# Kernel optimization log

Measured on AMD Instinct MI355X. Metric: run time of the kernel, lower is better.

The kernel has to match this reference:

```python
import jax, jax.numpy as jnp
import numpy as np

B, C, H, W = 4, 512, 64, 64
C8 = C // 8


def setup_inputs() -> dict:
    key = jax.random.key(0)
    ks = jax.random.split(key, 5)
    s1 = 1.0 / np.sqrt(C)
    return {
        "feat_map": jax.random.normal(ks[0], (B, C, H, W), jnp.float32),
        "w1": jax.random.normal(ks[1], (C8, C), jnp.float32) * s1,
        "b1": jnp.zeros((C8,), jnp.float32),
        "w2": jax.random.normal(ks[2], (C8, C), jnp.float32) * s1,
        "b2": jnp.zeros((C8,), jnp.float32),
        "w3": jax.random.normal(ks[3], (C, C), jnp.float32) * s1,
        "b3": jnp.zeros((C,), jnp.float32),
        "gamma": jax.random.normal(ks[4], (1,), jnp.float32) * 0.1,
    }


def reference(feat_map, w1, b1, w2, b2, w3, b3, gamma):
    b, c, h, w = feat_map.shape
    n = h * w
    x = feat_map.reshape(b, c, n)  # [B,C,N]
    # 1x1 convs are channel-mixing GEMMs
    q = jnp.einsum('kc,bcn->bnk', w1, x) + b1[None, None, :]   # [B,N,C8]
    k = jnp.einsum('kc,bcn->bkn', w2, x) + b2[None, :, None]   # [B,C8,N]
    v = jnp.einsum('dc,bcn->bdn', w3, x) + b3[None, :, None]   # [B,C,N]
    relation = jnp.einsum('bik,bkj->bij', q, k)                # [B,N,N]
    attn = jax.nn.softmax(relation, axis=-1)                   # softmax over keys j
    # feat_refine[b,c,i] = sum_j v[b,c,j] * attn[b,i,j]
    refine = jnp.einsum('bdj,bij->bdi', v, attn)               # [B,C,N]
    out = gamma[0] * refine.reshape(b, c, h, w) + feat_map
    return out
```

## Files before the change

### kernel.cpp

```cpp
#include <hip/hip_runtime.h>
#include <hip/hip_bf16.h>

typedef __attribute__((ext_vector_type(8))) short bf16x8_t;
typedef __attribute__((ext_vector_type(4))) float f32x4_t;

#define B_   4
#define C_   512
#define N_   4096
#define NQK_ 128
#define NT_  128
#define NP_  64

typedef unsigned short ushort_t;

__device__ __forceinline__ ushort_t f2bf(float f) {
    union { float f; unsigned int u; } un; un.f = f;
    unsigned int r = un.u + 0x7FFF + ((un.u >> 16) & 1);
    return (ushort_t)(r >> 16);
}

__device__ __forceinline__ bf16x8_t load8(const ushort_t* p) {
    return *reinterpret_cast<const bf16x8_t*>(p);
}

__device__ __forceinline__ unsigned pk2(float lo, float hi) {
    return (unsigned)f2bf(lo) | ((unsigned)f2bf(hi) << 16);
}

#define GLL16(g, l) __builtin_amdgcn_global_load_lds( \
    (const __attribute__((address_space(1))) unsigned int*)(g), \
    (__attribute__((address_space(3))) unsigned int*)(l), 16, 0, 0)

__global__ __launch_bounds__(256) void transpose_cast_x(
        const float* __restrict__ x, ushort_t* __restrict__ Xt,
        const float* __restrict__ w1, const float* __restrict__ b1,
        const float* __restrict__ w2, const float* __restrict__ b2,
        const float* __restrict__ w3, const float* __restrict__ b3,
        ushort_t* __restrict__ Wb, float* __restrict__ bias_all) {
    if (blockIdx.z == 4) {
        int bid = blockIdx.y * 64 + blockIdx.x;
        int t0 = bid * 256 + threadIdx.x;
        for (int idx = t0; idx < 640 * 512 + 640; idx += 131072) {
            if (idx < 64 * 512) {
                Wb[idx] = f2bf(w1[idx]);
            } else if (idx < 128 * 512) {
                Wb[idx] = f2bf(w2[idx - 64 * 512]);
            } else if (idx < 640 * 512) {
                Wb[idx] = f2bf(w3[idx - 128 * 512]);
            } else {
                int i = idx - 640 * 512;
                bias_all[i] = (i < 64) ? b1[i] : (i < 128 ? b2[i - 64] : b3[i - 128]);
            }
        }
        return;
    }
    int b = blockIdx.z, c0 = blockIdx.y * 64, n0 = blockIdx.x * 64;
    int tid = threadIdx.x;
    __shared__ float t[64][65];
    const float* xb = x + ((size_t)b * C_ + c0) * N_ + n0;
    #pragma unroll
    for (int it = 0; it < 4; ++it) {
        int cl = it * 16 + (tid >> 4), nq = (tid & 15) * 4;
        const float4 v = *reinterpret_cast<const float4*>(xb + (size_t)cl * N_ + nq);
        t[cl][nq + 0] = v.x; t[cl][nq + 1] = v.y;
        t[cl][nq + 2] = v.z; t[cl][nq + 3] = v.w;
    }
    __syncthreads();
    #pragma unroll
    for (int it = 0; it < 4; ++it) {
        int nl = it * 16 + (tid >> 4), cq = (tid & 15) * 4;
        ushort4 o;
        o.x = f2bf(t[cq + 0][nl]); o.y = f2bf(t[cq + 1][nl]);
        o.z = f2bf(t[cq + 2][nl]); o.w = f2bf(t[cq + 3][nl]);
        *reinterpret_cast<ushort4*>(&Xt[((size_t)b * N_ + n0 + nl) * C_ + c0 + cq]) = o;
    }
}

__global__ __launch_bounds__(256) void gemm_qkv_kernel(
        const ushort_t* __restrict__ Xt, const ushort_t* __restrict__ Wb,
        const float* __restrict__ bias, ushort_t* __restrict__ QK,
        ushort_t* __restrict__ V) {
    int sel = blockIdx.y;
    int n0 = blockIdx.x * 128;
    int tid = threadIdx.x;
    int l = tid & 63, w = tid >> 6;
    int wr = w >> 1, wc = w & 1;
    int lr = l & 15, lg = l >> 4;
    if (sel < 4) {
        int b = sel;
        const ushort_t* Xb = Xt + (size_t)b * N_ * C_;
        const ushort_t* ap = Xb + (size_t)(n0 + wr * 64 + lr) * 512 + lg * 8;
        const ushort_t* bp = Wb + (size_t)(wc * 64 + lr) * 512 + lg * 8;
        f32x4_t acc[4][4] = {};
        bf16x8_t a[4], bb[4];
        #pragma unroll
        for (int f = 0; f < 4; ++f) {
            a[f]  = load8(ap + (size_t)f * 16 * 512);
            bb[f] = load8(bp + (size_t)f * 16 * 512);
        }
        for (int kk = 0; kk < 512; kk += 32) {
            bf16x8_t na[4], nbb[4];
            if (kk + 32 < 512) {
                #pragma unroll
                for (int f = 0; f < 4; ++f) {
                    na[f]  = load8(ap + (size_t)f * 16 * 512 + kk + 32);
                    nbb[f] = load8(bp + (size_t)f * 16 * 512 + kk + 32);
                }
            }
            #pragma unroll
            for (int fi = 0; fi < 4; ++fi)
                #pragma unroll
                for (int fj = 0; fj < 4; ++fj)
                    acc[fi][fj] = __builtin_amdgcn_mfma_f32_16x16x32_bf16(
                        a[fi], bb[fj], acc[fi][fj], 0, 0, 0);
            if (kk + 32 < 512) {
                #pragma unroll
                for (int f = 0; f < 4; ++f) { a[f] = na[f]; bb[f] = nbb[f]; }
            }
        }
        #pragma unroll
        for (int fi = 0; fi < 4; ++fi)
            #pragma unroll
            for (int fj = 0; fj < 4; ++fj)
                #pragma unroll
                for (int r = 0; r < 4; ++r) {
                    int n = n0 + wr * 64 + fi * 16 + lg * 4 + r;
                    int col = wc * 64 + fj * 16 + lr;
                    QK[((size_t)b * N_ + n) * NQK_ + col] = f2bf(acc[fi][fj][r] + bias[col]);
                }
    } else {
        int m0 = ((sel - 4) & 3) * 128;
        int b  = (sel - 4) >> 2;
        const ushort_t* Xb = Xt + (size_t)b * N_ * C_;
        const ushort_t* Wv = Wb + 128 * 512;
        const ushort_t* ap = Wv + (size_t)(m0 + wr * 64 + lr) * 512 + lg * 8;
        const ushort_t* bp = Xb + (size_t)(n0 + wc * 64 + lr) * 512 + lg * 8;
        f32x4_t acc[4][4] = {};
        bf16x8_t a[4], bb[4];
        #pragma unroll
        for (int f = 0; f < 4; ++f) {
            a[f]  = load8(ap + (size_t)f * 16 * 512);
            bb[f] = load8(bp + (size_t)f * 16 * 512);
        }
        for (int kk = 0; kk < 512; kk += 32) {
            bf16x8_t na[4], nbb[4];
            if (kk + 32 < 512) {
                #pragma unroll
                for (int f = 0; f < 4; ++f) {
                    na[f]  = load8(ap + (size_t)f * 16 * 512 + kk + 32);
                    nbb[f] = load8(bp + (size_t)f * 16 * 512 + kk + 32);
                }
            }
            #pragma unroll
            for (int fi = 0; fi < 4; ++fi)
                #pragma unroll
                for (int fj = 0; fj < 4; ++fj)
                    acc[fi][fj] = __builtin_amdgcn_mfma_f32_16x16x32_bf16(
                        a[fi], bb[fj], acc[fi][fj], 0, 0, 0);
            if (kk + 32 < 512) {
                #pragma unroll
                for (int f = 0; f < 4; ++f) { a[f] = na[f]; bb[f] = nbb[f]; }
            }
        }
        #pragma unroll
        for (int fi = 0; fi < 4; ++fi)
            #pragma unroll
            for (int fj = 0; fj < 4; ++fj)
                #pragma unroll
                for (int r = 0; r < 4; ++r) {
                    int d = m0 + wr * 64 + fi * 16 + lg * 4 + r;
                    int n = n0 + wc * 64 + fj * 16 + lr;
                    V[((size_t)b * C_ + d) * N_ + n] = f2bf(acc[fi][fj][r] + bias[128 + d]);
                }
    }
}

__global__ __launch_bounds__(768, 3) void attn_kernel(
        const ushort_t* __restrict__ QK, const ushort_t* __restrict__ V,
        const float* __restrict__ feat, const float* __restrict__ gamma,
        float* __restrict__ out) {
    __shared__ ushort_t Vl[3][16384];
    __shared__ ushort_t Kl3[3][4096];
    __shared__ ushort_t Pl[2][4096];
    __shared__ float    fl[2][128];
    __shared__ __align__(16) unsigned flagl[2][8];
    __shared__ float    invl[64];

    int bid = blockIdx.x;
    int lid = (bid & 7) * 32 + (bid >> 3);
    int b  = lid >> 6;
    int i0 = (lid & 63) * 64;

    int tid = threadIdx.x;
    int l = tid & 63, w = tid >> 6;
    int lr = l & 15, lg = l >> 4;
    int ds = (w >= 4) ? (w - 4) : 0;

    const ushort_t* QKb = QK + (size_t)b * N_ * NQK_;
    const ushort_t* Vb  = V  + (size_t)b * C_ * N_;

    bf16x8_t qf0 = {}, qf1 = {};
    const ushort_t* ksrc = nullptr;
    float mreg = -1e30f, ssum = 0.0f;
    const int maskk = (lr & 7) << 4;
    if (w < 4) {
        qf0 = load8(QKb + (size_t)(i0 + w * 16 + lr) * NQK_ + lg * 8);
        qf1 = load8(QKb + (size_t)(i0 + w * 16 + lr) * NQK_ + 32 + lg * 8);
        int p = w * 1024 + l * 16;
        int o = p ^ (((p >> 7) & 7) << 4);
        ksrc = QKb + (size_t)(o >> 7) * NQK_ + 64 + ((o & 127) >> 1);
    }

    int cst = (l & 7) ^ (l >> 3);
    const ushort_t* vsrc = Vb + (size_t)(ds * 64 + 2 * (l >> 3) + (cst >> 2)) * N_
                              + (cst & 3) * 8;
    int c2 = ((lr & 1) * 4 + lg) ^ (lr >> 1);
    const int vread = ds * 2048 + (lr >> 1) * 64 + c2 * 8;
    f32x4_t acc[4][4] = {};

    if (w < 4) {
        GLL16(ksrc,                         &Kl3[0][w * 512]);
        GLL16(ksrc + (size_t)1 * 32 * NQK_, &Kl3[0][2048 + w * 512]);
        GLL16(ksrc + (size_t)2 * 32 * NQK_, &Kl3[1][w * 512]);
        GLL16(ksrc + (size_t)3 * 32 * NQK_, &Kl3[1][2048 + w * 512]);
        asm volatile("s_waitcnt vmcnt(2)" ::: "memory");
    } else {
        #pragma unroll
        for (int h = 0; h < 4; ++h)
            GLL16(vsrc + (size_t)h * 16 * N_,      &Vl[0][ds * 2048 + h * 512]);
        #pragma unroll
        for (int h = 0; h < 4; ++h)
            GLL16(vsrc + (size_t)h * 16 * N_ + 32, &Vl[1][ds * 2048 + h * 512]);
        #pragma unroll
        for (int h = 0; h < 4; ++h)
            GLL16(vsrc + (size_t)h * 16 * N_ + 64, &Vl[2][ds * 2048 + h * 512]);
    }
    asm volatile("" ::: "memory");
    __builtin_amdgcn_s_barrier();
    asm volatile("" ::: "memory");

#define SOFTMAX_WRITE(SO0, SO1, PM, TT)                                        \
    {                                                                          \
        float pmax = fmaxf(fmaxf(fmaxf(SO0[0],SO0[1]), fmaxf(SO0[2],SO0[3])),  \
                           fmaxf(fmaxf(SO1[0],SO1[1]), fmaxf(SO1[2],SO1[3]))); \
        pmax = fmaxf(pmax, __shfl_xor(pmax, 16));                              \
        pmax = fmaxf(pmax, __shfl_xor(pmax, 32));                              \
        bool anyneed = __any(pmax > mreg + 8.0f);                              \
        if (anyneed) {                                                         \
            float mn = fmaxf(mreg, pmax);                                      \
            float f_ = __expf(mreg - mn);                                      \
            mreg = mn; ssum *= f_;                                             \
            if (lg == 0) fl[PM][(TT) * 64 + w * 16 + lr] = f_;                 \
        }                                                                      \
        if (l == 0) flagl[PM][(TT) * 4 + w] = anyneed ? 1u : 0u;               \
        float e00 = __expf(SO0[0]-mreg), e01 = __expf(SO0[1]-mreg);            \
        float e02 = __expf(SO0[2]-mreg), e03 = __expf(SO0[3]-mreg);            \
        float e10 = __expf(SO1[0]-mreg), e11 = __expf(SO1[1]-mreg);            \
        float e12 = __expf(SO1[2]-mreg), e13 = __expf(SO1[3]-mreg);            \
        ssum += (e00+e01)+(e02+e03)+(e10+e11)+(e12+e13);    \
        int lt = lr + (lg >> 1) * 16;                                          \
        uint2 w0v; w0v.x = pk2(e00, e01); w0v.y = pk2(e02, e03);               \
        uint2 w1v; w1v.x = pk2(e10, e11); w1v.y = pk2(e12, e13);               \
        *reinterpret_cast<uint2*>(&Pl[PM][(TT)*2048 + w*512 + lt*8 + (lg&1)*4]) = w0v; \
        *reinterpret_cast<uint2*>(&Pl[PM][(TT)*2048 + w*512 + (lt+32)*8 + (lg&1)*4]) = w1v; \
    }

#define PVSTEP(PB, TT, VB, STJ, DOSTAGE)                                       \
    {                                                                          \
        bf16x8_t vf[4];                                                        \
        _Pragma("unroll") for (int dt = 0; dt < 4; ++dt)                       \
            vf[dt] = load8(&Vl[VB][vread + dt * 512]);                         \
        asm volatile("s_waitcnt lgkmcnt(0)" ::: "memory");                     \
        if (DOSTAGE) {                                                         \
            const ushort_t* vsT = vsrc + (STJ) * 32;                           \
            _Pragma("unroll") for (int h = 0; h < 4; ++h)                      \
                GLL16(vsT + (size_t)h * 16 * N_, &Vl[VB][ds * 2048 + h * 512]); \
        }                                                                      \
        uint4 fv = *reinterpret_cast<const uint4*>(&flagl[PB][(TT) * 4]);      \
        if ((int)__builtin_amdgcn_readfirstlane(fv.x)) {                       \
            float fq = fl[PB][(TT) * 64 + lr];                                 \
            _Pragma("unroll") for (int dt = 0; dt < 4; ++dt) acc[dt][0] *= fq; \
        }                                                                      \
        if ((int)__builtin_amdgcn_readfirstlane(fv.y)) {                       \
            float fq = fl[PB][(TT) * 64 + 16 + lr];                            \
            _Pragma("unroll") for (int dt = 0; dt < 4; ++dt) acc[dt][1] *= fq; \
        }                                                                      \
        if ((int)__builtin_amdgcn_readfirstlane(fv.z)) {                       \
            float fq = fl[PB][(TT) * 64 + 32 + lr];                            \
            _Pragma("unroll") for (int dt = 0; dt < 4; ++dt) acc[dt][2] *= fq; \
        }                                                                      \
        if ((int)__builtin_amdgcn_readfirstlane(fv.w)) {                       \
            float fq = fl[PB][(TT) * 64 + 48 + lr];                            \
            _Pragma("unroll") for (int dt = 0; dt < 4; ++dt) acc[dt][3] *= fq; \
        }                                                                      \
        __builtin_amdgcn_s_setprio(1);                                         \
        _Pragma("unroll") for (int qt = 0; qt < 4; ++qt) {                     \
            bf16x8_t pa = load8(&Pl[PB][(TT) * 2048 + qt * 512 + l * 8]);      \
            _Pragma("unroll") for (int dt = 0; dt < 4; ++dt)                   \
                acc[dt][qt] = __builtin_amdgcn_mfma_f32_16x16x32_bf16(         \
                    vf[dt], pa, acc[dt][qt], 0, 0, 0);                         \
        }                                                                      \
        __builtin_amdgcn_s_setprio(0);                                         \
    }

    for (int p = 0; p < NP_; ++p) {
        int pb = p % 3;
        if (w < 4) {
            if (p + 2 < NP_) {
                int pn = pb + 2; if (pn >= 3) pn -= 3;
                GLL16(ksrc + (size_t)(2 * p + 4) * 32 * NQK_, &Kl3[pn][w * 512]);
                GLL16(ksrc + (size_t)(2 * p + 5) * 32 * NQK_, &Kl3[pn][2048 + w * 512]);
            }
            const ushort_t* kbp = &Kl3[pb][0];
            bf16x8_t kf00, kf01, kf10, kf11;
            { int o = (lr << 7) + (lg << 4);              kf00 = load8(kbp + ((o ^ maskk) >> 1)); }
            { int o = (lr << 7) + 64 + (lg << 4);         kf01 = load8(kbp + ((o ^ maskk) >> 1)); }
            { int o = ((16 + lr) << 7) + (lg << 4);       kf10 = load8(kbp + ((o ^ maskk) >> 1)); }
            { int o = ((16 + lr) << 7) + 64 + (lg << 4);  kf11 = load8(kbp + ((o ^ maskk) >> 1)); }
            f32x4_t s00 = {0.f,0.f,0.f,0.f}, s01 = {0.f,0.f,0.f,0.f};
            s00 = __builtin_amdgcn_mfma_f32_16x16x32_bf16(kf00, qf0, s00, 0,0,0);
            s00 = __builtin_amdgcn_mfma_f32_16x16x32_bf16(kf01, qf1, s00, 0,0,0);
            s01 = __builtin_amdgcn_mfma_f32_16x16x32_bf16(kf10, qf0, s01, 0,0,0);
            s01 = __builtin_amdgcn_mfma_f32_16x16x32_bf16(kf11, qf1, s01, 0,0,0);
            const ushort_t* kbq = kbp + 2048;
            bf16x8_t kg00, kg01, kg10, kg11;
            { int o = (lr << 7) + (lg << 4);              kg00 = load8(kbq + ((o ^ maskk) >> 1)); }
            { int o = (lr << 7) + 64 + (lg << 4);         kg01 = load8(kbq + ((o ^ maskk) >> 1)); }
            { int o = ((16 + lr) << 7) + (lg << 4);       kg10 = load8(kbq + ((o ^ maskk) >> 1)); }
            { int o = ((16 + lr) << 7) + 64 + (lg << 4);  kg11 = load8(kbq + ((o ^ maskk) >> 1)); }
            f32x4_t s10 = {0.f,0.f,0.f,0.f}, s11 = {0.f,0.f,0.f,0.f};
            s10 = __builtin_amdgcn_mfma_f32_16x16x32_bf16(kg00, qf0, s10, 0,0,0);
            s10 = __builtin_amdgcn_mfma_f32_16x16x32_bf16(kg01, qf1, s10, 0,0,0);
            s11 = __builtin_amdgcn_mfma_f32_16x16x32_bf16(kg10, qf0, s11, 0,0,0);
            s11 = __builtin_amdgcn_mfma_f32_16x16x32_bf16(kg11, qf1, s11, 0,0,0);
            int bank = p & 1;
            SOFTMAX_WRITE(s00, s01, bank, 0)
            SOFTMAX_WRITE(s10, s11, bank, 1)
            asm volatile("s_waitcnt vmcnt(2) lgkmcnt(0)" ::: "memory");
        } else {
            if (p >= 1) {
                int pbk = (p - 1) & 1;
                int j0 = 2 * p - 2, j1 = 2 * p - 1;
                PVSTEP(pbk, 0, j0 % 3, j0 + 3, (j0 + 3 < NT_))
                PVSTEP(pbk, 1, j1 % 3, j1 + 3, (j1 + 3 < NT_))
            }
            asm volatile("s_waitcnt vmcnt(4)" ::: "memory");
        }
        asm volatile("" ::: "memory");
        __builtin_amdgcn_s_barrier();
        asm volatile("" ::: "memory");
    }

    if (w < 4) {
        ssum += __shfl_xor(ssum, 16);
        ssum += __shfl_xor(ssum, 32);
        if (lg == 0) invl[w * 16 + lr] = 1.0f / ssum;
        asm volatile("s_waitcnt lgkmcnt(0)" ::: "memory");
    } else {
        asm volatile("s_waitcnt vmcnt(0)" ::: "memory");
    }
    asm volatile("" ::: "memory");
    __builtin_amdgcn_s_barrier();
    asm volatile("" ::: "memory");

    if (w >= 4) {
        PVSTEP(1, 0, 0, 0, false)
        PVSTEP(1, 1, 1, 0, false)
        asm volatile("s_waitcnt lgkmcnt(0)" ::: "memory");

        float g = gamma[0];
        float iq0 = invl[lr], iq1 = invl[16 + lr], iq2 = invl[32 + lr], iq3 = invl[48 + lr];
        #pragma unroll
        for (int dt = 0; dt < 4; ++dt) {
            #pragma unroll
            for (int r = 0; r < 4; ++r) {
                size_t row = ((size_t)b * C_ + ds * 64 + dt * 16 + lg * 4 + r) * N_;
                size_t i0r = row + i0;
                { size_t idx = i0r + lr;      out[idx] = g * acc[dt][0][r] * iq0 + feat[idx]; }
                { size_t idx = i0r + 16 + lr; out[idx] = g * acc[dt][1][r] * iq1 + feat[idx]; }
                { size_t idx = i0r + 32 + lr; out[idx] = g * acc[dt][2][r] * iq2 + feat[idx]; }
                { size_t idx = i0r + 48 + lr; out[idx] = g * acc[dt][3][r] * iq3 + feat[idx]; }
            }
        }
    }
#undef PVSTEP
#undef SOFTMAX_WRITE
}

extern "C" void kernel_launch(void* const* d_in, const int* in_sizes, int n_in,
                              void* d_out, int out_size, void* d_ws, size_t ws_size,
                              hipStream_t stream) {
    const float* feat  = (const float*)d_in[0];
    const float* w1    = (const float*)d_in[1];
    const float* b1    = (const float*)d_in[2];
    const float* w2    = (const float*)d_in[3];
    const float* b2    = (const float*)d_in[4];
    const float* w3    = (const float*)d_in[5];
    const float* b3    = (const float*)d_in[6];
    const float* gamma = (const float*)d_in[7];
    float* out = (float*)d_out;

    char* ws = (char*)d_ws;
    ushort_t* Xt      = (ushort_t*)(ws);
    ushort_t* Wb      = (ushort_t*)(ws + 16777216);
    float*    biasAll = (float*)   (ws + 17432576);
    ushort_t* QKp     = (ushort_t*)(ws + 17435136);
    ushort_t* Vp      = (ushort_t*)(ws + 21629440);
    if (ws_size < 38406656) return;

    hipLaunchKernelGGL(transpose_cast_x, dim3(64, 8, 5), dim3(256), 0, stream,
                       feat, Xt, w1, b1, w2, b2, w3, b3, Wb, biasAll);
    hipLaunchKernelGGL(gemm_qkv_kernel, dim3(32, 20), dim3(256), 0, stream,
                       Xt, Wb, biasAll, QKp, Vp);
    hipLaunchKernelGGL(attn_kernel, dim3(256), dim3(768), 0, stream,
                       QKp, Vp, feat, gamma, out);
}
```

Baseline: 165.4 us.

## Load V fragments directly into registers instead of staging through LDS

Removes the triple-buffered V shared-memory staging (96KB of LDS). PV warps now load V MFMA operands straight from global memory into registers, double-buffered as even and odd tiles, with vmcnt waits and sched_barriers placed before each PV step. This drops LDS writes and reads and frees a large share of LDS, which may allow more blocks to be resident. In exchange, the global loads now use a row-strided pattern with 16-byte accesses per lane, which could lower coalescing and expose global latency to the MFMA chain.

```diff
diff --git a/kernel.cpp b/kernel.cpp
--- a/kernel.cpp
+++ b/kernel.cpp
@@ -179,7 +179,6 @@
         const ushort_t* __restrict__ QK, const ushort_t* __restrict__ V,
         const float* __restrict__ feat, const float* __restrict__ gamma,
         float* __restrict__ out) {
-    __shared__ ushort_t Vl[3][16384];
     __shared__ ushort_t Kl3[3][4096];
     __shared__ ushort_t Pl[2][4096];
     __shared__ float    fl[2][128];
@@ -211,12 +210,18 @@
         ksrc = QKb + (size_t)(o >> 7) * NQK_ + 64 + ((o & 127) >> 1);
     }
 
-    int cst = (l & 7) ^ (l >> 3);
-    const ushort_t* vsrc = Vb + (size_t)(ds * 64 + 2 * (l >> 3) + (cst >> 2)) * N_
-                              + (cst & 3) * 8;
-    int c2 = ((lr & 1) * 4 + lg) ^ (lr >> 1);
-    const int vread = ds * 2048 + (lr >> 1) * 64 + c2 * 8;
+    const ushort_t* vgE = Vb + (size_t)(ds * 64 + lr) * N_ + lg * 8;
+    const ushort_t* vgO = vgE + 32;
+    bf16x8_t E0, E1, E2, E3, O0, O1, O2, O3;
     f32x4_t acc[4][4] = {};
+
+#define VLOAD(D, P) asm volatile("global_load_dwordx4 %0, %1, off" \
+        : "=v"(D) : "v"(P) : "memory")
+#define VFETCH4(A0, A1, A2, A3, P)                   \
+    VLOAD(A0, (P));                                  \
+    VLOAD(A1, (P) + (size_t)16 * N_);                \
+    VLOAD(A2, (P) + (size_t)32 * N_);                \
+    VLOAD(A3, (P) + (size_t)48 * N_);
 
     if (w < 4) {
         GLL16(ksrc,                         &Kl3[0][w * 512]);
@@ -225,15 +230,10 @@
         GLL16(ksrc + (size_t)3 * 32 * NQK_, &Kl3[1][2048 + w * 512]);
         asm volatile("s_waitcnt vmcnt(2)" ::: "memory");
     } else {
-        #pragma unroll
-        for (int h = 0; h < 4; ++h)
-            GLL16(vsrc + (size_t)h * 16 * N_,      &Vl[0][ds * 2048 + h * 512]);
-        #pragma unroll
-        for (int h = 0; h < 4; ++h)
-            GLL16(vsrc + (size_t)h * 16 * N_ + 32, &Vl[1][ds * 2048 + h * 512]);
-        #pragma unroll
-        for (int h = 0; h < 4; ++h)
-            GLL16(vsrc + (size_t)h * 16 * N_ + 64, &Vl[2][ds * 2048 + h * 512]);
+        VFETCH4(E0, E1, E2, E3, vgE)
+        vgE += 64;
+        VFETCH4(O0, O1, O2, O3, vgO)
+        vgO += 64;
     }
     asm volatile("" ::: "memory");
     __builtin_amdgcn_s_barrier();
@@ -265,17 +265,8 @@
         *reinterpret_cast<uint2*>(&Pl[PM][(TT)*2048 + w*512 + (lt+32)*8 + (lg&1)*4]) = w1v; \
     }
 
-#define PVSTEP(PB, TT, VB, STJ, DOSTAGE)                                       \
+#define PVSTEP_R(PB, TT, V0, V1, V2, V3)                                       \
     {                                                                          \
-        bf16x8_t vf[4];                                                        \
-        _Pragma("unroll") for (int dt = 0; dt < 4; ++dt)                       \
-            vf[dt] = load8(&Vl[VB][vread + dt * 512]);                         \
-        asm volatile("s_waitcnt lgkmcnt(0)" ::: "memory");                     \
-        if (DOSTAGE) {                                                         \
-            const ushort_t* vsT = vsrc + (STJ) * 32;                           \
-            _Pragma("unroll") for (int h = 0; h < 4; ++h)                      \
-                GLL16(vsT + (size_t)h * 16 * N_, &Vl[VB][ds * 2048 + h * 512]); \
-        }                                                                      \
         uint4 fv = *reinterpret_cast<const uint4*>(&flagl[PB][(TT) * 4]);      \
         if ((int)__builtin_amdgcn_readfirstlane(fv.x)) {                       \
             float fq = fl[PB][(TT) * 64 + lr];                                 \
@@ -296,9 +287,14 @@
         __builtin_amdgcn_s_setprio(1);                                         \
         _Pragma("unroll") for (int qt = 0; qt < 4; ++qt) {                     \
             bf16x8_t pa = load8(&Pl[PB][(TT) * 2048 + qt * 512 + l * 8]);      \
-            _Pragma("unroll") for (int dt = 0; dt < 4; ++dt)                   \
-                acc[dt][qt] = __builtin_amdgcn_mfma_f32_16x16x32_bf16(         \
-                    vf[dt], pa, acc[dt][qt], 0, 0, 0);                         \
+            acc[0][qt] = __builtin_amdgcn_mfma_f32_16x16x32_bf16(              \
+                V0, pa, acc[0][qt], 0, 0, 0);                                  \
+            acc[1][qt] = __builtin_amdgcn_mfma_f32_16x16x32_bf16(              \
+                V1, pa, acc[1][qt], 0, 0, 0);                                  \
+            acc[2][qt] = __builtin_amdgcn_mfma_f32_16x16x32_bf16(              \
+                V2, pa, acc[2][qt], 0, 0, 0);                                  \
+            acc[3][qt] = __builtin_amdgcn_mfma_f32_16x16x32_bf16(              \
+                V3, pa, acc[3][qt], 0, 0, 0);                                  \
         }                                                                      \
         __builtin_amdgcn_s_setprio(0);                                         \
     }
@@ -340,11 +336,17 @@
         } else {
             if (p >= 1) {
                 int pbk = (p - 1) & 1;
-                int j0 = 2 * p - 2, j1 = 2 * p - 1;
-                PVSTEP(pbk, 0, j0 % 3, j0 + 3, (j0 + 3 < NT_))
-                PVSTEP(pbk, 1, j1 % 3, j1 + 3, (j1 + 3 < NT_))
-            }
-            asm volatile("s_waitcnt vmcnt(4)" ::: "memory");
+                asm volatile("s_waitcnt vmcnt(4)" ::: "memory");
+                __builtin_amdgcn_sched_barrier(0);
+                PVSTEP_R(pbk, 0, E0, E1, E2, E3)
+                VFETCH4(E0, E1, E2, E3, vgE)
+                vgE += 64;
+                asm volatile("s_waitcnt vmcnt(4)" ::: "memory");
+                __builtin_amdgcn_sched_barrier(0);
+                PVSTEP_R(pbk, 1, O0, O1, O2, O3)
+                VFETCH4(O0, O1, O2, O3, vgO)
+                vgO += 64;
+            }
         }
         asm volatile("" ::: "memory");
         __builtin_amdgcn_s_barrier();
@@ -356,17 +358,18 @@
         ssum += __shfl_xor(ssum, 32);
         if (lg == 0) invl[w * 16 + lr] = 1.0f / ssum;
         asm volatile("s_waitcnt lgkmcnt(0)" ::: "memory");
-    } else {
-        asm volatile("s_waitcnt vmcnt(0)" ::: "memory");
     }
     asm volatile("" ::: "memory");
     __builtin_amdgcn_s_barrier();
     asm volatile("" ::: "memory");
 
     if (w >= 4) {
-        PVSTEP(1, 0, 0, 0, false)
-        PVSTEP(1, 1, 1, 0, false)
-        asm volatile("s_waitcnt lgkmcnt(0)" ::: "memory");
+        asm volatile("s_waitcnt vmcnt(4)" ::: "memory");
+        __builtin_amdgcn_sched_barrier(0);
+        PVSTEP_R(1, 0, E0, E1, E2, E3)
+        asm volatile("s_waitcnt vmcnt(0)" ::: "memory");
+        __builtin_amdgcn_sched_barrier(0);
+        PVSTEP_R(1, 1, O0, O1, O2, O3)
 
         float g = gamma[0];
         float iq0 = invl[lr], iq1 = invl[16 + lr], iq2 = invl[32 + lr], iq3 = invl[48 + lr];
@@ -383,8 +386,10 @@
             }
         }
     }
-#undef PVSTEP
+#undef PVSTEP_R
 #undef SOFTMAX_WRITE
+#undef VFETCH4
+#undef VLOAD
 }
 
 extern "C" void kernel_launch(void* const* d_in, const int* in_sizes, int n_in,
```

New measurement: 189.6 us. 14.6% more time.

## Stage QKV GEMM operands through double-buffered LDS with direct global-to-LDS loads

Applied to the files above, without the earlier changes.

The QKV projection GEMM now loads A and B tiles cooperatively into double-buffered shared memory using global-to-LDS loads (GLL16), with explicit vmcnt waits and barriers. Previously each wave loaded its own fragments straight from global memory, so tiles were fetched redundantly across waves. The two branches are unified into one shared main loop. The change adds two barriers per k-step and extra LDS traffic in exchange for less duplicated global memory traffic.

```diff
diff --git a/kernel.cpp b/kernel.cpp
--- a/kernel.cpp
+++ b/kernel.cpp
@@ -80,44 +80,70 @@
         const ushort_t* __restrict__ Xt, const ushort_t* __restrict__ Wb,
         const float* __restrict__ bias, ushort_t* __restrict__ QK,
         ushort_t* __restrict__ V) {
+    __shared__ ushort_t Al[2][4096];
+    __shared__ ushort_t Bl[2][4096];
     int sel = blockIdx.y;
     int n0 = blockIdx.x * 128;
     int tid = threadIdx.x;
     int l = tid & 63, w = tid >> 6;
     int wr = w >> 1, wc = w & 1;
     int lr = l & 15, lg = l >> 4;
+
+    int m0 = 0, bV = 0;
+    const ushort_t* asrc;
+    const ushort_t* bsrc;
     if (sel < 4) {
-        int b = sel;
-        const ushort_t* Xb = Xt + (size_t)b * N_ * C_;
-        const ushort_t* ap = Xb + (size_t)(n0 + wr * 64 + lr) * 512 + lg * 8;
-        const ushort_t* bp = Wb + (size_t)(wc * 64 + lr) * 512 + lg * 8;
-        f32x4_t acc[4][4] = {};
-        bf16x8_t a[4], bb[4];
+        asrc = Xt + ((size_t)sel * N_ + n0) * 512;
+        bsrc = Wb;
+    } else {
+        m0 = ((sel - 4) & 3) * 128;
+        bV = (sel - 4) >> 2;
+        asrc = Wb + (size_t)(128 + m0) * 512;
+        bsrc = Xt + ((size_t)bV * N_ + n0) * 512;
+    }
+    const ushort_t* ast = asrc + (size_t)(l >> 2) * 512 + (l & 3) * 8;
+    const ushort_t* bst = bsrc + (size_t)(l >> 2) * 512 + (l & 3) * 8;
+
+#define STAGEK(BUF, K0)                                                        \
+    {                                                                          \
+        GLL16(ast + (size_t)(w * 32) * 512 + (K0),      &Al[BUF][w * 1024]);       \
+        GLL16(ast + (size_t)(w * 32 + 16) * 512 + (K0), &Al[BUF][w * 1024 + 512]); \
+        GLL16(bst + (size_t)(w * 32) * 512 + (K0),      &Bl[BUF][w * 1024]);       \
+        GLL16(bst + (size_t)(w * 32 + 16) * 512 + (K0), &Bl[BUF][w * 1024 + 512]); \
+    }
+
+    f32x4_t acc[4][4] = {};
+    STAGEK(0, 0)
+    for (int i = 0; i < 16; ++i) {
+        int cur = i & 1;
+        if (i < 15) {
+            STAGEK(cur ^ 1, (i + 1) * 32)
+            asm volatile("s_waitcnt vmcnt(4)" ::: "memory");
+        } else {
+            asm volatile("s_waitcnt vmcnt(0)" ::: "memory");
+        }
+        asm volatile("" ::: "memory");
+        __builtin_amdgcn_s_barrier();
+        asm volatile("" ::: "memory");
+        bf16x8_t a[4], b8[4];
         #pragma unroll
         for (int f = 0; f < 4; ++f) {
-            a[f]  = load8(ap + (size_t)f * 16 * 512);
-            bb[f] = load8(bp + (size_t)f * 16 * 512);
+            a[f]  = load8(&Al[cur][(wr * 64 + f * 16 + lr) * 32 + lg * 8]);
+            b8[f] = load8(&Bl[cur][(wc * 64 + f * 16 + lr) * 32 + lg * 8]);
         }
-        for (int kk = 0; kk < 512; kk += 32) {
-            bf16x8_t na[4], nbb[4];
-            if (kk + 32 < 512) {
-                #pragma unroll
-                for (int f = 0; f < 4; ++f) {
-                    na[f]  = load8(ap + (size_t)f * 16 * 512 + kk + 32);
-                    nbb[f] = load8(bp + (size_t)f * 16 * 512 + kk + 32);
-                }
-            }
+        #pragma unroll
+        for (int fi = 0; fi < 4; ++fi)
             #pragma unroll
-            for (int fi = 0; fi < 4; ++fi)
-                #pragma unroll
-                for (int fj = 0; fj < 4; ++fj)
-                    acc[fi][fj] = __builtin_amdgcn_mfma_f32_16x16x32_bf16(
-                        a[fi], bb[fj], acc[fi][fj], 0, 0, 0);
-            if (kk + 32 < 512) {
-                #pragma unroll
-                for (int f = 0; f < 4; ++f) { a[f] = na[f]; bb[f] = nbb[f]; }
-            }
-        }
+            for (int fj = 0; fj < 4; ++fj)
+                acc[fi][fj] = __builtin_amdgcn_mfma_f32_16x16x32_bf16(
+                    a[fi], b8[fj], acc[fi][fj], 0, 0, 0);
+        asm volatile("" ::: "memory");
+        __builtin_amdgcn_s_barrier();
+        asm volatile("" ::: "memory");
+    }
+#undef STAGEK
+
+    if (sel < 4) {
         #pragma unroll
         for (int fi = 0; fi < 4; ++fi)
             #pragma unroll
@@ -126,42 +152,9 @@
                 for (int r = 0; r < 4; ++r) {
                     int n = n0 + wr * 64 + fi * 16 + lg * 4 + r;
                     int col = wc * 64 + fj * 16 + lr;
-                    QK[((size_t)b * N_ + n) * NQK_ + col] = f2bf(acc[fi][fj][r] + bias[col]);
+                    QK[((size_t)sel * N_ + n) * NQK_ + col] = f2bf(acc[fi][fj][r] + bias[col]);
                 }
     } else {
-        int m0 = ((sel - 4) & 3) * 128;
-        int b  = (sel - 4) >> 2;
-        const ushort_t* Xb = Xt + (size_t)b * N_ * C_;
-        const ushort_t* Wv = Wb + 128 * 512;
-        const ushort_t* ap = Wv + (size_t)(m0 + wr * 64 + lr) * 512 + lg * 8;
-        const ushort_t* bp = Xb + (size_t)(n0 + wc * 64 + lr) * 512 + lg * 8;
-        f32x4_t acc[4][4] = {};
-        bf16x8_t a[4], bb[4];
-        #pragma unroll
-        for (int f = 0; f < 4; ++f) {
-            a[f]  = load8(ap + (size_t)f * 16 * 512);
-            bb[f] = load8(bp + (size_t)f * 16 * 512);
-        }
-        for (int kk = 0; kk < 512; kk += 32) {
-            bf16x8_t na[4], nbb[4];
-            if (kk + 32 < 512) {
-                #pragma unroll
-                for (int f = 0; f < 4; ++f) {
-                    na[f]  = load8(ap + (size_t)f * 16 * 512 + kk + 32);
-                    nbb[f] = load8(bp + (size_t)f * 16 * 512 + kk + 32);
-                }
-            }
-            #pragma unroll
-            for (int fi = 0; fi < 4; ++fi)
-                #pragma unroll
-                for (int fj = 0; fj < 4; ++fj)
-                    acc[fi][fj] = __builtin_amdgcn_mfma_f32_16x16x32_bf16(
-                        a[fi], bb[fj], acc[fi][fj], 0, 0, 0);
-            if (kk + 32 < 512) {
-                #pragma unroll
-                for (int f = 0; f < 4; ++f) { a[f] = na[f]; bb[f] = nbb[f]; }
-            }
-        }
         #pragma unroll
         for (int fi = 0; fi < 4; ++fi)
             #pragma unroll
@@ -170,7 +163,7 @@
                 for (int r = 0; r < 4; ++r) {
                     int d = m0 + wr * 64 + fi * 16 + lg * 4 + r;
                     int n = n0 + wc * 64 + fj * 16 + lr;
-                    V[((size_t)b * C_ + d) * N_ + n] = f2bf(acc[fi][fj][r] + bias[128 + d]);
+                    V[((size_t)bV * C_ + d) * N_ + n] = f2bf(acc[fi][fj][r] + bias[128 + d]);
                 }
     }
 }
```

New measurement: 139.7 us. 1.18x faster.
